# Optimization experiments

Hardware: AMD Instinct MI355X
Metric: run time of the kernel (lower is better)

Reference implementation:

```python
import jax, jax.numpy as jnp
import numpy as np

J, T, N_VARS, K = 64, 64, 4, 8   # n_inputs, terms per input poly, vars, Bernstein coeffs per var
I = 64                            # layer_size (output nodes)


def setup_inputs() -> dict:
    key = jax.random.key(0)
    k1, k2, k3, k4, k5, k6 = jax.random.split(key, 6)
    return {
        "layer_inputs_under": jax.random.normal(k1, (J, T, N_VARS, K), jnp.float32),
        "layer_inputs_over": jax.random.normal(k2, (J, T, N_VARS, K), jnp.float32),
        "layer_inputs_under_degrees": jax.random.randint(k3, (J, N_VARS), 0, 5).astype(jnp.float32),
        "layer_inputs_over_degrees": jax.random.randint(k4, (J, N_VARS), 0, 5).astype(jnp.float32),
        "layer_weights": jax.random.normal(k5, (I, J), jnp.float32),
        "layer_biases": jax.random.normal(k6, (I,), jnp.float32),
    }


def _scale_polys(polys, w):
    """mult_with_constant, vectorized over nodes and inputs.
    In IBF a polynomial is scaled by a constant by scaling the FIRST variable's
    coefficient row of every term.  polys: [J,T,n,k], w: [I,J] -> [I,J,T,n,k]."""
    i = w.shape[0]
    row0 = polys[None, :, :, 0:1, :] * w[:, :, None, None, None]        # [I,J,T,1,k]
    rest = jnp.broadcast_to(polys[None, :, :, 1:, :],
                            (i, polys.shape[0], polys.shape[1], polys.shape[2] - 1, polys.shape[3]))
    return jnp.concatenate([row0, rest], axis=3)


def _layer(liu, lio, w, b):
    """LayerModule.forward with activation='linear' (identity path of NodeModule).
    node_under = sum_j (w_neg[i,j]*over_j + w_pos[i,j]*under_j) + bias term
    node_over  = sum_j (w_pos[i,j]*over_j + w_neg[i,j]*under_j) + bias term
    sum_2_polys == concatenation of term lists; add_with_constant appends one
    constant term (row0 = bias, remaining variable rows = ones)."""
    w_pos = jax.nn.relu(w)
    w_neg = -jax.nn.relu(-w)
    j, t, n, k = liu.shape
    i = w.shape[0]

    def combine(wa, wb):
        pa = _scale_polys(lio, wa).reshape(i, j * t, n, k)  # scaled over-polys
        pb = _scale_polys(liu, wb).reshape(i, j * t, n, k)  # scaled under-polys
        return jnp.concatenate([pa, pb], axis=1)            # [I, 2JT, n, k]

    under = combine(w_neg, w_pos)
    over = combine(w_pos, w_neg)

    bias_term = jnp.concatenate(
        [b[:, None, None, None] * jnp.ones((i, 1, 1, k), b.dtype),
         jnp.ones((i, 1, n - 1, k), b.dtype)], axis=2)      # [I,1,n,k]
    under = jnp.concatenate([under, bias_term], axis=1)     # [I, 2JT+1, n, k]
    over = jnp.concatenate([over, bias_term], axis=1)
    return under, over


def reference(layer_inputs_under, layer_inputs_over, layer_inputs_under_degrees,
              layer_inputs_over_degrees, layer_weights, layer_biases):
    under, over = _layer(layer_inputs_under, layer_inputs_over, layer_weights, layer_biases)
    # degree of each node poly = elementwise max of contributing input degrees
    deg = jnp.maximum(layer_inputs_under_degrees, layer_inputs_over_degrees).max(axis=0)  # [n]
    i = layer_weights.shape[0]
    under_deg = jnp.broadcast_to(deg, (i, deg.shape[0]))
    over_deg = under_deg
    return under, over, under_deg, over_deg
```

## Files before the change

kernel.cpp:

```cpp
#include <hip/hip_runtime.h>

namespace {
constexpr int Jc = 64, Tc = 64, NVc = 4, Ic = 64;
constexpr int F4_TERM  = 8;
constexpr int TERMS    = 2 * Jc * Tc + 1;
constexpr int NODE_F4  = TERMS * F4_TERM;
constexpr int TILE_F4  = Tc * F4_TERM;
constexpr long long SIDE_F4 = (long long)Ic * NODE_F4;
constexpr long long DEG_BASE_FLT = 2LL * SIDE_F4 * 4;
constexpr int CHUNK_F4 = 2048;
constexpr int CHUNKS   = 32;
}

typedef float v4f __attribute__((ext_vector_type(4)));

__device__ __forceinline__ void nt_store4(float4* p, float x, float y, float z, float w) {
    v4f v = {x, y, z, w};
    __builtin_nontemporal_store(v, reinterpret_cast<v4f*>(p));
}

__global__ __launch_bounds__(256) void layer_kernel(
    const float4* __restrict__ liu,
    const float4* __restrict__ lio,
    const float*  __restrict__ ud,
    const float*  __restrict__ od,
    const float*  __restrict__ w,
    const float*  __restrict__ bias,
    float*        __restrict__ outf)
{
    float4* out = reinterpret_cast<float4*>(outf);
    const int b   = blockIdx.x;
    const int tid = (int)threadIdx.x;

    if (b < Ic * 2 * CHUNKS) {
        const int c = b & (CHUNKS - 1);
        const int s = (b >> 5) & 1;
        const int i = b >> 6;

        float4* dst = out + (long long)s * SIDE_F4 + (long long)i * NODE_F4
                          + (long long)c * CHUNK_F4;

        #pragma unroll
        for (int jr = 0; jr < 4; ++jr) {
            const int jj   = c * 4 + jr;
            const int half = jj >> 6;
            const int j    = jj & 63;
            const float wv = w[i * Jc + j];
            const float wp = fmaxf(wv, 0.0f);
            const float wn = fminf(wv, 0.0f);
            const float sv0 = (half == s) ? wn : wp;
            const float4* src = (half ? liu : lio) + j * TILE_F4;
            #pragma unroll
            for (int h = 0; h < 2; ++h) {
                const int idx = h * 256 + tid;
                const float4 v = src[idx];
                const float sc = ((idx & 7) < 2) ? sv0 : 1.0f;
                nt_store4(dst + jr * 512 + idx, v.x * sc, v.y * sc, v.z * sc, v.w * sc);
            }
        }
    } else {
        #pragma unroll
        for (int r = 0; r < 4; ++r) {
            const int t    = r * 256 + tid;
            const int reg  = t >> 3;
            const int i    = reg >> 1;
            const int s    = reg & 1;
            const int sub  = t & 7;
            const float val = (sub < 2) ? bias[i] : 1.0f;
            const long long off = (long long)s * SIDE_F4 + (long long)i * NODE_F4
                                  + (long long)(2 * Jc * Tc) * F4_TERM + sub;
            nt_store4(out + off, val, val, val, val);
        }
        const int var = tid & 3;
        float m = -3.4e38f;
        for (int j = 0; j < Jc; ++j) {
            m = fmaxf(m, fmaxf(ud[j * NVc + var], od[j * NVc + var]));
        }
        outf[DEG_BASE_FLT + tid] = m;
        outf[DEG_BASE_FLT + 256 + tid] = m;
    }
}

extern "C" void kernel_launch(void* const* d_in, const int* in_sizes, int n_in,
                              void* d_out, int out_size, void* d_ws, size_t ws_size,
                              hipStream_t stream) {
    const float4* liu  = (const float4*)d_in[0];
    const float4* lio  = (const float4*)d_in[1];
    const float*  ud   = (const float*)d_in[2];
    const float*  od   = (const float*)d_in[3];
    const float*  w    = (const float*)d_in[4];
    const float*  bias = (const float*)d_in[5];
    float* outf = (float*)d_out;

    layer_kernel<<<dim3(Ic * 2 * CHUNKS + 1), dim3(256), 0, stream>>>(
        liu, lio, ud, od, w, bias, outf);
}
```

Measured before the change: 155.0 us.

## Reuse each loaded input tile across eight output nodes per block

Each block now loads one input polynomial tile once and writes it, scaled, to eight output nodes, instead of reloading the source for every node. This cuts global reads by a factor of eight and changes the block decomposition to 2048 blocks that each issue sixteen stores. The degree reduction in the tail block also becomes a wavefront shuffle reduction instead of a serial 64-step loop. The kernel is dominated by the output write stream, so the read savings may matter little, and the changed store pattern strides across nodes.

Result: faster. 147.8 us (-4.7%).

```diff
diff --git a/kernel.cpp b/kernel.cpp
--- a/kernel.cpp
+++ b/kernel.cpp
@@ -8,8 +8,8 @@
 constexpr int TILE_F4  = Tc * F4_TERM;
 constexpr long long SIDE_F4 = (long long)Ic * NODE_F4;
 constexpr long long DEG_BASE_FLT = 2LL * SIDE_F4 * 4;
-constexpr int CHUNK_F4 = 2048;
-constexpr int CHUNKS   = 32;
+constexpr int IG = 8;
+constexpr int MAIN_BLOCKS = 2 * 2 * Jc * (Ic / IG);
 }
 
 typedef float v4f __attribute__((ext_vector_type(4)));
@@ -32,31 +32,36 @@
     const int b   = blockIdx.x;
     const int tid = (int)threadIdx.x;
 
-    if (b < Ic * 2 * CHUNKS) {
-        const int c = b & (CHUNKS - 1);
-        const int s = (b >> 5) & 1;
-        const int i = b >> 6;
+    if (b < MAIN_BLOCKS) {
+        const int ig = b & 7;
+        const int jj = (b >> 3) & 127;
+        const int s  = b >> 10;
+        const int h  = jj >> 6;
+        const int j  = jj & 63;
+        const int i0 = ig * IG;
 
-        float4* dst = out + (long long)s * SIDE_F4 + (long long)i * NODE_F4
-                          + (long long)c * CHUNK_F4;
+        const float4* src = (h ? liu : lio) + j * TILE_F4;
+        const float4 va = src[tid];
+        const float4 vb = src[tid + 256];
+        const bool isv0 = (tid & 7) < 2;
 
+        float sv[IG];
         #pragma unroll
-        for (int jr = 0; jr < 4; ++jr) {
-            const int jj   = c * 4 + jr;
-            const int half = jj >> 6;
-            const int j    = jj & 63;
-            const float wv = w[i * Jc + j];
+        for (int t = 0; t < IG; ++t) {
+            const float wv = w[(i0 + t) * Jc + j];
             const float wp = fmaxf(wv, 0.0f);
             const float wn = fminf(wv, 0.0f);
-            const float sv0 = (half == s) ? wn : wp;
-            const float4* src = (half ? liu : lio) + j * TILE_F4;
-            #pragma unroll
-            for (int h = 0; h < 2; ++h) {
-                const int idx = h * 256 + tid;
-                const float4 v = src[idx];
-                const float sc = ((idx & 7) < 2) ? sv0 : 1.0f;
-                nt_store4(dst + jr * 512 + idx, v.x * sc, v.y * sc, v.z * sc, v.w * sc);
-            }
+            sv[t] = (h == s) ? wn : wp;
+        }
+
+        float4* dst = out + (long long)s * SIDE_F4 + (long long)i0 * NODE_F4
+                          + (long long)jj * TILE_F4 + tid;
+        #pragma unroll
+        for (int t = 0; t < IG; ++t) {
+            const float sc = isv0 ? sv[t] : 1.0f;
+            nt_store4(dst,       va.x * sc, va.y * sc, va.z * sc, va.w * sc);
+            nt_store4(dst + 256, vb.x * sc, vb.y * sc, vb.z * sc, vb.w * sc);
+            dst += NODE_F4;
         }
     } else {
         #pragma unroll
@@ -71,13 +76,20 @@
                                   + (long long)(2 * Jc * Tc) * F4_TERM + sub;
             nt_store4(out + off, val, val, val, val);
         }
-        const int var = tid & 3;
-        float m = -3.4e38f;
-        for (int j = 0; j < Jc; ++j) {
-            m = fmaxf(m, fmaxf(ud[j * NVc + var], od[j * NVc + var]));
+        const int lane = tid & 63;
+        float m[NVc];
+        #pragma unroll
+        for (int v = 0; v < NVc; ++v)
+            m[v] = fmaxf(ud[lane * NVc + v], od[lane * NVc + v]);
+        #pragma unroll
+        for (int mask = 1; mask < 64; mask <<= 1) {
+            #pragma unroll
+            for (int v = 0; v < NVc; ++v)
+                m[v] = fmaxf(m[v], __shfl_xor(m[v], mask, 64));
         }
-        outf[DEG_BASE_FLT + tid] = m;
-        outf[DEG_BASE_FLT + 256 + tid] = m;
+        const float dv = m[tid & 3];
+        outf[DEG_BASE_FLT + tid] = dv;
+        outf[DEG_BASE_FLT + 256 + tid] = dv;
     }
 }
 
@@ -92,6 +104,6 @@
     const float*  bias = (const float*)d_in[5];
     float* outf = (float*)d_out;
 
-    layer_kernel<<<dim3(Ic * 2 * CHUNKS + 1), dim3(256), 0, stream>>>(
+    layer_kernel<<<dim3(MAIN_BLOCKS + 1), dim3(256), 0, stream>>>(
         liu, lio, ud, od, w, bias, outf);
 }
```
